# Performance work log

Measured on AMD Instinct MI355X. Metric: run time of the kernel, lower is better.

The kernel has to match this reference:

```python
import jax, jax.numpy as jnp
import numpy as np


def setup_inputs() -> dict:
    key = jax.random.key(0)
    ks = jax.random.split(key, 6)
    B, S, C, D, E, EMB = 512, 512, 32, 512, 8, 32
    x = jax.random.normal(ks[0], (B, S, C), dtype=jnp.float32)
    Wp = jax.random.normal(ks[1], (C, D), dtype=jnp.float32) / np.sqrt(C)
    bp = jnp.zeros((D,), dtype=jnp.float32)
    emb = jax.random.normal(ks[2], (E, EMB), dtype=jnp.float32)
    Wg = jax.random.normal(ks[3], (D + EMB,), dtype=jnp.float32) / np.sqrt(D + EMB)
    bg = jnp.zeros((1,), dtype=jnp.float32)
    We = jax.random.normal(ks[4], (E, S, D), dtype=jnp.float32) / np.sqrt(S)
    return {"x": x, "Wp": Wp, "bp": bp, "emb": emb, "Wg": Wg, "bg": bg,
            "We": We, "k": 2}


def reference(x, Wp, bp, emb, Wg, bg, We, k):
    # x: [B, S, C]  (batch, seq_len, enc_in)
    B, S, C = x.shape
    E = We.shape[0]
    # RevIN 'subtract_median' normalization along the sequence dim
    xn = x - jnp.median(x, axis=1, keepdims=True)  # [B, S, C]
    # gating context from the last timestep, projected to d_model
    ctx = xn[:, -1, :] @ Wp + bp                    # [B, D]
    # condition gate on expert-identity embeddings: concat([ctx, emb_e])
    feat = jnp.concatenate(
        [jnp.broadcast_to(ctx[:, None, :], (B, E, ctx.shape[-1])),
         jnp.broadcast_to(emb[None, :, :], (B, E, emb.shape[-1]))],
        axis=-1)                                    # [B, E, D+EMB]
    clean_logits = feat @ Wg + bg[0]                # [B, E]
    # top-k gating (eval path: no noise), softmax over the k selected logits
    top_v, top_i = jax.lax.top_k(clean_logits, k)   # [B, k]
    top_g = jax.nn.softmax(top_v, axis=-1)          # [B, k]
    gates = jnp.zeros((B, E), dtype=x.dtype)
    gates = gates.at[jnp.arange(B)[:, None], top_i].set(top_g)  # sparse [B, E]
    # per-expert linear along seq: expert e maps [S, C] -> [D, C]
    expert_out = jnp.einsum('bsv,esd->ebdv', xn, We)  # [E, B, D, C]
    # weighted scatter-combine (equals SparseDispatcher.combine since
    # gates are zero outside the top-k set)
    combined = jnp.einsum('be,ebdv->bdv', gates, expert_out)  # [B, D, C]
    return combined
```

## Files before the change

kernel.cpp:

```cpp
#include <hip/hip_runtime.h>

typedef unsigned int u32;
typedef unsigned short u16;
typedef unsigned long long u64;
typedef float f32x4 __attribute__((ext_vector_type(4)));
typedef short s16x8 __attribute__((ext_vector_type(8)));

#define Bn 512
#define Sn 512
#define Cn 32
#define Dn 512

__device__ __forceinline__ u32 f2bf(float f) {
  u32 u = __float_as_uint(f);
  return (u + 0x7FFFu + ((u >> 16) & 1u)) >> 16;
}
__device__ __forceinline__ float bfl(u32 p) { return __uint_as_float(p << 16); }
__device__ __forceinline__ float bfh(u32 p) { return __uint_as_float(p & 0xFFFF0000u); }

__device__ __forceinline__ float keyToFloat(u32 k) {
  u32 u = (k & 0x80000000u) ? (k ^ 0x80000000u) : ~k;
  return __uint_as_float(u);
}

__device__ __forceinline__ int xtIdx(int v, int k) {
  return v * 64 + ((((k >> 3) ^ (v & 7))) << 2) + ((k & 7) >> 1);
}

__global__ void k_gates(const float* __restrict__ emb, const float* __restrict__ Wg,
                        float* __restrict__ gbuf) {
  int t = threadIdx.x;
  __shared__ float ed[8];
  if (t < 8) {
    float s = 0.f;
#pragma unroll
    for (int j = 0; j < 32; ++j) s += emb[t * 32 + j] * Wg[Dn + j];
    ed[t] = s;
  }
  __syncthreads();
  if (t == 0) {
    int i1 = 0;
#pragma unroll
    for (int e = 1; e < 8; ++e) if (ed[e] > ed[i1]) i1 = e;
    int i2 = (i1 == 0) ? 1 : 0;
#pragma unroll
    for (int e = 0; e < 8; ++e) if (e != i1 && ed[e] > ed[i2]) i2 = e;
    float a = ed[i1], b = ed[i2];
    float m = fmaxf(a, b);
    float ea = __expf(a - m), eb = __expf(b - m);
    float inv = 1.f / (ea + eb);
    gbuf[0] = ea * inv;
    gbuf[1] = eb * inv;
    ((int*)gbuf)[2] = i1;
    ((int*)gbuf)[3] = i2;
  }
}

__global__ __launch_bounds__(256) void k_wmix(const float* __restrict__ We,
                                              const float* __restrict__ gbuf,
                                              u16* __restrict__ WmT) {
  __shared__ float tile[64][65];
  int bi = blockIdx.x;
  int sb = (bi & 7) * 64, db = (bi >> 3) * 64;
  float g1 = gbuf[0], g2 = gbuf[1];
  int e1 = ((const int*)gbuf)[2], e2 = ((const int*)gbuf)[3];
  const float* W1 = We + (size_t)e1 * Sn * Dn;
  const float* W2 = We + (size_t)e2 * Sn * Dn;
  int t = threadIdx.x;
#pragma unroll
  for (int i = 0; i < 16; ++i) {
    int idx = t + i * 256;
    int sl = idx >> 6, dl = idx & 63;
    int g = (sb + sl) * Dn + db + dl;
    tile[sl][dl] = g1 * W1[g] + g2 * W2[g];
  }
  __syncthreads();
#pragma unroll
  for (int i = 0; i < 16; ++i) {
    int idx = t + i * 256;
    int dl = idx >> 6, sl = idx & 63;
    WmT[(size_t)(db + dl) * Sn + sb + sl] = (u16)f2bf(tile[sl][dl]);
  }
}

__global__ void k_colsum(const u16* __restrict__ WmT, float* __restrict__ colsum) {
  int d = blockIdx.x, l = threadIdx.x;
  const uint4* p = (const uint4*)(WmT + (size_t)d * Sn + l * 8);
  uint4 u = *p;
  float s = bfl(u.x) + bfh(u.x) + bfl(u.y) + bfh(u.y) +
            bfl(u.z) + bfh(u.z) + bfl(u.w) + bfh(u.w);
#pragma unroll
  for (int off = 32; off >= 1; off >>= 1) s += __shfl_xor(s, off, 64);
  if (l == 0) colsum[d] = s;
}

__global__ __launch_bounds__(256) void k_median(const float* __restrict__ x,
                                                float* __restrict__ med) {
  __shared__ float buf[64][20];
  int blk = blockIdx.x;
  int b = blk >> 1, half = blk & 1;
  int t = threadIdx.x;
  int w = t >> 6, l = t & 63;
  u32 K[4][8];
  const float4* xb = (const float4*)(x + (size_t)b * Sn * Cn);
#pragma unroll
  for (int sc = 0; sc < 8; ++sc) {
    {
      int sl = t >> 2, vq = t & 3;
      float4 f = xb[(sc * 64 + sl) * 8 + half * 4 + vq];
      *(float4*)&buf[sl][vq * 4] = f;
    }
    __syncthreads();
#pragma unroll
    for (int cc = 0; cc < 4; ++cc) {
      u32 u = __float_as_uint(buf[l][w * 4 + cc]);
      K[cc][sc] = (u >> 31) ? ~u : (u | 0x80000000u);
    }
    __syncthreads();
  }
  int base = b * 32 + half * 16 + w * 4;
#pragma unroll
  for (int cc = 0; cc < 4; ++cc) {
    u32 a1 = 0;
#pragma unroll
    for (int bit = 31; bit >= 0; --bit) {
      u32 cand = a1 | (1u << bit);
      int c = 0;
#pragma unroll
      for (int j = 0; j < 8; ++j) c += __popcll(__ballot(K[cc][j] < cand));
      if (c <= 255) a1 = cand;
    }
    int cle = 0;
#pragma unroll
    for (int j = 0; j < 8; ++j) cle += __popcll(__ballot(K[cc][j] <= a1));
    u32 a2;
    if (cle >= 257) {
      a2 = a1;
    } else {
      u32 mn = 0xFFFFFFFFu;
#pragma unroll
      for (int j = 0; j < 8; ++j) {
        u32 k2 = K[cc][j];
        if (k2 > a1 && k2 < mn) mn = k2;
      }
      mn = min(mn, (u32)__shfl_xor((int)mn, 1, 64));
      mn = min(mn, (u32)__shfl_xor((int)mn, 2, 64));
      mn = min(mn, (u32)__shfl_xor((int)mn, 4, 64));
      mn = min(mn, (u32)__shfl_xor((int)mn, 8, 64));
      mn = min(mn, (u32)__shfl_xor((int)mn, 16, 64));
      mn = min(mn, (u32)__shfl_xor((int)mn, 32, 64));
      a2 = mn;
    }
    if (l == 0) med[base + cc] = 0.5f * (keyToFloat(a1) + keyToFloat(a2));
  }
}

__global__ __launch_bounds__(256) void k_gemm(const float* __restrict__ x,
                                              const u16* __restrict__ WmT,
                                              const float* __restrict__ med,
                                              const float* __restrict__ colsum,
                                              float* __restrict__ out) {
  __shared__ __align__(16) u32 xT[32 * 128 / 2];
  int b = blockIdx.x;
  int t = threadIdx.x;
  int w = t >> 6, l = t & 63;
  int q = l >> 4, col = l & 15;
  int dw = w * 128;
  f32x4 acc[8][2] = {};
  const float* xb = x + (size_t)b * Sn * Cn;
#pragma unroll 1
  for (int ch = 0; ch < 4; ++ch) {
    int s0 = ch * 128;
#pragma unroll
    for (int i = 0; i < 2; ++i) {
      int u = t + i * 256;
      int sp = u >> 3, vq = u & 7;
      int sl = sp * 2;
      const float4* pa = (const float4*)(xb + (size_t)(s0 + sl) * Cn) + vq;
      float4 fa = pa[0];
      float4 fb = pa[8];
#pragma unroll
      for (int j = 0; j < 4; ++j) {
        int v = vq * 4 + j;
        u32 pk = f2bf((&fa.x)[j]) | (f2bf((&fb.x)[j]) << 16);
        xT[xtIdx(v, sl)] = pk;
      }
    }
    __syncthreads();
#pragma unroll
    for (int kk = 0; kk < 4; ++kk) {
      s16x8 bf[2];
#pragma unroll
      for (int nt = 0; nt < 2; ++nt) {
        int v = col + nt * 16;
        int k = kk * 32 + q * 8;
        bf[nt] = *(const s16x8*)&xT[xtIdx(v, k)];
      }
#pragma unroll
      for (int mt = 0; mt < 8; ++mt) {
        int d = dw + mt * 16 + col;
        const s16x8* ap =
            (const s16x8*)(WmT + (size_t)d * Sn + ch * 128 + kk * 32 + q * 8);
        s16x8 af = *ap;
        acc[mt][0] = __builtin_amdgcn_mfma_f32_16x16x32_bf16(af, bf[0], acc[mt][0], 0, 0, 0);
        acc[mt][1] = __builtin_amdgcn_mfma_f32_16x16x32_bf16(af, bf[1], acc[mt][1], 0, 0, 0);
      }
    }
    __syncthreads();
  }
  float m0 = med[b * 32 + col];
  float m1 = med[b * 32 + 16 + col];
  float* ob = out + (size_t)b * Dn * Cn;
#pragma unroll
  for (int mt = 0; mt < 8; ++mt) {
#pragma unroll
    for (int r = 0; r < 4; ++r) {
      int d = dw + mt * 16 + q * 4 + r;
      float cs = colsum[d];
      ob[d * 32 + col]      = acc[mt][0][r] - m0 * cs;
      ob[d * 32 + 16 + col] = acc[mt][1][r] - m1 * cs;
    }
  }
}

extern "C" void kernel_launch(void* const* d_in, const int* in_sizes, int n_in,
                              void* d_out, int out_size, void* d_ws, size_t ws_size,
                              hipStream_t stream) {
  const float* x   = (const float*)d_in[0];
  const float* emb = (const float*)d_in[3];
  const float* Wg  = (const float*)d_in[4];
  const float* We  = (const float*)d_in[6];
  float* out = (float*)d_out;
  char* ws = (char*)d_ws;
  float* gbuf   = (float*)(ws);
  float* colsum = (float*)(ws + 256);
  float* med    = (float*)(ws + 4096);
  u16*   WmT    = (u16*)(ws + 4096 + 65536);

  hipLaunchKernelGGL(k_gates,  dim3(1),    dim3(64),  0, stream, emb, Wg, gbuf);
  hipLaunchKernelGGL(k_wmix,   dim3(64),   dim3(256), 0, stream, We, gbuf, WmT);
  hipLaunchKernelGGL(k_colsum, dim3(512),  dim3(64),  0, stream, WmT, colsum);
  hipLaunchKernelGGL(k_median, dim3(1024), dim3(256), 0, stream, x, med);
  hipLaunchKernelGGL(k_gemm,   dim3(512),  dim3(256), 0, stream, x, WmT, med, colsum, out);
}
```

Baseline: 166.9 us.

## Pre-transpose x to bf16 in median kernel and retile GEMM with LDS staging

The median kernel now loads a whole batch slice into LDS at once and also writes a transposed bf16 copy of x ([B*C, S]). The GEMM is restructured as a 128x128 tile GEMM over (D) x (B*C), using direct global-to-LDS loads with an XOR swizzle for both operands and 4x4 MFMA tiles per wave. This replaces per-batch blocks that reread the mixed weights from global memory and converted x in-kernel. In exchange it adds an extra bf16 round trip of x through memory and makes the epilogue stores strided.

```diff
diff --git a/kernel.cpp b/kernel.cpp
--- a/kernel.cpp
+++ b/kernel.cpp
@@ -2,7 +2,6 @@
 
 typedef unsigned int u32;
 typedef unsigned short u16;
-typedef unsigned long long u64;
 typedef float f32x4 __attribute__((ext_vector_type(4)));
 typedef short s16x8 __attribute__((ext_vector_type(8)));
 
@@ -17,14 +16,14 @@
 }
 __device__ __forceinline__ float bfl(u32 p) { return __uint_as_float(p << 16); }
 __device__ __forceinline__ float bfh(u32 p) { return __uint_as_float(p & 0xFFFF0000u); }
-
 __device__ __forceinline__ float keyToFloat(u32 k) {
   u32 u = (k & 0x80000000u) ? (k ^ 0x80000000u) : ~k;
   return __uint_as_float(u);
 }
-
-__device__ __forceinline__ int xtIdx(int v, int k) {
-  return v * 64 + ((((k >> 3) ^ (v & 7))) << 2) + ((k & 7) >> 1);
+__device__ __forceinline__ void gl2lds16(const void* g, void* l) {
+  __builtin_amdgcn_global_load_lds(
+      (const __attribute__((address_space(1))) u32*)g,
+      (__attribute__((address_space(3))) u32*)l, 16, 0, 0);
 }
 
 __global__ void k_gates(const float* __restrict__ emb, const float* __restrict__ Wg,
@@ -94,31 +93,52 @@
   if (l == 0) colsum[d] = s;
 }
 
-__global__ __launch_bounds__(256) void k_median(const float* __restrict__ x,
-                                                float* __restrict__ med) {
-  __shared__ float buf[64][20];
+__global__ __launch_bounds__(256) void k_prep(const float* __restrict__ x,
+                                              float* __restrict__ med,
+                                              u16* __restrict__ xbf) {
+  __shared__ float buf[512][17];
   int blk = blockIdx.x;
   int b = blk >> 1, half = blk & 1;
+  int vbase = half * 16;
   int t = threadIdx.x;
   int w = t >> 6, l = t & 63;
+  const float4* xb4 = (const float4*)(x + (size_t)b * Sn * Cn);
+  float4 f[8];
+#pragma unroll
+  for (int i = 0; i < 8; ++i)
+    f[i] = xb4[((t >> 2) + i * 64) * 8 + half * 4 + (t & 3)];
+#pragma unroll
+  for (int i = 0; i < 8; ++i) {
+    int s = (t >> 2) + i * 64, c0 = (t & 3) * 4;
+    buf[s][c0 + 0] = f[i].x; buf[s][c0 + 1] = f[i].y;
+    buf[s][c0 + 2] = f[i].z; buf[s][c0 + 3] = f[i].w;
+  }
+  __syncthreads();
   u32 K[4][8];
-  const float4* xb = (const float4*)(x + (size_t)b * Sn * Cn);
-#pragma unroll
-  for (int sc = 0; sc < 8; ++sc) {
-    {
-      int sl = t >> 2, vq = t & 3;
-      float4 f = xb[(sc * 64 + sl) * 8 + half * 4 + vq];
-      *(float4*)&buf[sl][vq * 4] = f;
-    }
-    __syncthreads();
-#pragma unroll
-    for (int cc = 0; cc < 4; ++cc) {
-      u32 u = __float_as_uint(buf[l][w * 4 + cc]);
-      K[cc][sc] = (u >> 31) ? ~u : (u | 0x80000000u);
-    }
-    __syncthreads();
-  }
-  int base = b * 32 + half * 16 + w * 4;
+#pragma unroll
+  for (int cc = 0; cc < 4; ++cc)
+#pragma unroll
+    for (int j = 0; j < 8; ++j) {
+      u32 u = __float_as_uint(buf[j * 64 + l][w * 4 + cc]);
+      K[cc][j] = (u >> 31) ? ~u : (u | 0x80000000u);
+    }
+  {
+    int vl = t >> 4, sb = (t & 15) * 32;
+    u16* orow = xbf + ((size_t)(b * 32 + vbase + vl)) * Sn;
+#pragma unroll
+    for (int cq = 0; cq < 4; ++cq) {
+      int cp = (cq + (t & 15)) & 3;
+      u32 pk[4];
+#pragma unroll
+      for (int jj = 0; jj < 4; ++jj) {
+        u32 lo = f2bf(buf[sb + cp * 8 + jj * 2][vl]);
+        u32 hi = f2bf(buf[sb + cp * 8 + jj * 2 + 1][vl]);
+        pk[jj] = lo | (hi << 16);
+      }
+      *(uint4*)(orow + sb + cp * 8) = *(uint4*)pk;
+    }
+  }
+  int base = b * 32 + vbase + w * 4;
 #pragma unroll
   for (int cc = 0; cc < 4; ++cc) {
     u32 a1 = 0;
@@ -155,70 +175,69 @@
   }
 }
 
-__global__ __launch_bounds__(256) void k_gemm(const float* __restrict__ x,
-                                              const u16* __restrict__ WmT,
+__global__ __launch_bounds__(256) void k_gemm(const u16* __restrict__ WmT,
+                                              const u16* __restrict__ xbf,
                                               const float* __restrict__ med,
                                               const float* __restrict__ colsum,
                                               float* __restrict__ out) {
-  __shared__ __align__(16) u32 xT[32 * 128 / 2];
-  int b = blockIdx.x;
-  int t = threadIdx.x;
-  int w = t >> 6, l = t & 63;
-  int q = l >> 4, col = l & 15;
-  int dw = w * 128;
-  f32x4 acc[8][2] = {};
-  const float* xb = x + (size_t)b * Sn * Cn;
+  __shared__ __align__(16) u16 As[128 * 64];
+  __shared__ __align__(16) u16 Bs[128 * 64];
+  int bi = blockIdx.x;
+  int mb = bi & 3, nb = bi >> 2;
+  int t = threadIdx.x, w = t >> 6, l = t & 63;
+  int mh = (w & 1) * 64, nh = (w >> 1) * 64;
+  int lane16 = l & 15, q = l >> 4;
+  f32x4 acc[4][4] = {};
+  int r0 = t >> 3, c = t & 7;
+  const u16* Ab = WmT + (size_t)(mb * 128) * Sn;
+  const u16* Bb = xbf + (size_t)(nb * 128) * Sn;
 #pragma unroll 1
-  for (int ch = 0; ch < 4; ++ch) {
-    int s0 = ch * 128;
-#pragma unroll
-    for (int i = 0; i < 2; ++i) {
-      int u = t + i * 256;
-      int sp = u >> 3, vq = u & 7;
-      int sl = sp * 2;
-      const float4* pa = (const float4*)(xb + (size_t)(s0 + sl) * Cn) + vq;
-      float4 fa = pa[0];
-      float4 fb = pa[8];
-#pragma unroll
-      for (int j = 0; j < 4; ++j) {
-        int v = vq * 4 + j;
-        u32 pk = f2bf((&fa.x)[j]) | (f2bf((&fb.x)[j]) << 16);
-        xT[xtIdx(v, sl)] = pk;
-      }
+  for (int ch = 0; ch < 8; ++ch) {
+    int k0 = ch * 64;
+#pragma unroll
+    for (int i = 0; i < 4; ++i) {
+      int r = r0 + i * 32;
+      int gc = c ^ (r & 7);
+      gl2lds16(Ab + (size_t)r * Sn + k0 + gc * 8, (char*)As + t * 16 + i * 4096);
+      gl2lds16(Bb + (size_t)r * Sn + k0 + gc * 8, (char*)Bs + t * 16 + i * 4096);
     }
     __syncthreads();
 #pragma unroll
-    for (int kk = 0; kk < 4; ++kk) {
-      s16x8 bf[2];
-#pragma unroll
-      for (int nt = 0; nt < 2; ++nt) {
-        int v = col + nt * 16;
-        int k = kk * 32 + q * 8;
-        bf[nt] = *(const s16x8*)&xT[xtIdx(v, k)];
-      }
-#pragma unroll
-      for (int mt = 0; mt < 8; ++mt) {
-        int d = dw + mt * 16 + col;
-        const s16x8* ap =
-            (const s16x8*)(WmT + (size_t)d * Sn + ch * 128 + kk * 32 + q * 8);
-        s16x8 af = *ap;
-        acc[mt][0] = __builtin_amdgcn_mfma_f32_16x16x32_bf16(af, bf[0], acc[mt][0], 0, 0, 0);
-        acc[mt][1] = __builtin_amdgcn_mfma_f32_16x16x32_bf16(af, bf[1], acc[mt][1], 0, 0, 0);
-      }
+    for (int kk = 0; kk < 2; ++kk) {
+      s16x8 af[4], bf[4];
+#pragma unroll
+      for (int mt = 0; mt < 4; ++mt) {
+        int m = mh + mt * 16 + lane16;
+        int cs = (kk * 4 + q) ^ (m & 7);
+        af[mt] = *(const s16x8*)(As + m * 64 + cs * 8);
+      }
+#pragma unroll
+      for (int nt = 0; nt < 4; ++nt) {
+        int n = nh + nt * 16 + lane16;
+        int cs = (kk * 4 + q) ^ (n & 7);
+        bf[nt] = *(const s16x8*)(Bs + n * 64 + cs * 8);
+      }
+#pragma unroll
+      for (int mt = 0; mt < 4; ++mt)
+#pragma unroll
+        for (int nt = 0; nt < 4; ++nt)
+          acc[mt][nt] = __builtin_amdgcn_mfma_f32_16x16x32_bf16(af[mt], bf[nt], acc[mt][nt], 0, 0, 0);
     }
     __syncthreads();
   }
-  float m0 = med[b * 32 + col];
-  float m1 = med[b * 32 + 16 + col];
-  float* ob = out + (size_t)b * Dn * Cn;
-#pragma unroll
-  for (int mt = 0; mt < 8; ++mt) {
-#pragma unroll
-    for (int r = 0; r < 4; ++r) {
-      int d = dw + mt * 16 + q * 4 + r;
-      float cs = colsum[d];
-      ob[d * 32 + col]      = acc[mt][0][r] - m0 * cs;
-      ob[d * 32 + 16 + col] = acc[mt][1][r] - m1 * cs;
+#pragma unroll
+  for (int nt = 0; nt < 4; ++nt) {
+    int n = nb * 128 + nh + nt * 16 + lane16;
+    int b = n >> 5, v = n & 31;
+    float mv = med[n];
+    float* obase = out + (size_t)b * (Dn * Cn) + v;
+#pragma unroll
+    for (int mt = 0; mt < 4; ++mt) {
+      int d0 = mb * 128 + mh + mt * 16 + q * 4;
+      f32x4 cs = *(const f32x4*)(colsum + d0);
+#pragma unroll
+      for (int r = 0; r < 4; ++r)
+        obase[(size_t)(d0 + r) * Cn] = acc[mt][nt][r] - mv * cs[r];
     }
   }
 }
@@ -236,10 +255,11 @@
   float* colsum = (float*)(ws + 256);
   float* med    = (float*)(ws + 4096);
   u16*   WmT    = (u16*)(ws + 4096 + 65536);
+  u16*   xbf    = (u16*)(ws + 4096 + 65536 + 524288);
 
   hipLaunchKernelGGL(k_gates,  dim3(1),    dim3(64),  0, stream, emb, Wg, gbuf);
   hipLaunchKernelGGL(k_wmix,   dim3(64),   dim3(256), 0, stream, We, gbuf, WmT);
   hipLaunchKernelGGL(k_colsum, dim3(512),  dim3(64),  0, stream, WmT, colsum);
-  hipLaunchKernelGGL(k_median, dim3(1024), dim3(256), 0, stream, x, med);
-  hipLaunchKernelGGL(k_gemm,   dim3(512),  dim3(256), 0, stream, x, WmT, med, colsum, out);
-}
+  hipLaunchKernelGGL(k_prep,   dim3(1024), dim3(256), 0, stream, x, med, xbf);
+  hipLaunchKernelGGL(k_gemm,   dim3(512),  dim3(256), 0, stream, WmT, xbf, med, colsum, out);
+}
```

New measurement: 148.4 us. 1.12x faster.
